# Optimization experiments

Measured on AMD Instinct MI355X. Metric: run time of the kernel, lower is better.

The kernel has to match this reference:

```python
import jax, jax.numpy as jnp
import numpy as np

B = 256          # batchSize
KNEG = 4096      # K negatives
D = 128          # inputSize
N = 1000000      # outputSize (memory bank rows)
T = 0.07
MOM = 0.5
STDV = 1.0 / np.sqrt(D / 3.0)


def setup_inputs() -> dict:
    key = jax.random.key(0)
    k1, k2, k3, k4, k5, k6 = jax.random.split(key, 6)
    ab = jax.random.normal(k1, (B, D), dtype=jnp.float32)
    l = jax.random.normal(k2, (B, D), dtype=jnp.float32)
    ss = jax.random.normal(k3, (B, D), dtype=jnp.float32)
    # memory bank initialized uniform in [-stdv, stdv] like the torch buffer
    memory_ab = jax.random.uniform(k4, (N, D), dtype=jnp.float32) * (2 * STDV) - STDV
    idx = jax.random.randint(k5, (B, KNEG + 1), 0, N)
    y = jax.random.randint(k6, (B,), 0, N)
    idx = idx.at[:, 0].set(y)  # positive sample in column 0
    return {"ab": ab, "l": l, "ss": ss, "memory_ab": memory_ab,
            "idx": idx, "y": y}


def reference(ab, l, ss, memory_ab, idx, y):
    # gather: [B, K+1, D]; detached in the original (no grad to the bank)
    w = jax.lax.stop_gradient(memory_ab[idx])
    # three batched dot-product scores against the same gathered weights
    out_l = jnp.einsum('bkd,bd->bk', w, l)[..., None] / T
    out_ss = jnp.einsum('bkd,bd->bk', w, ss)[..., None] / T
    out_orig = jnp.einsum('bkd,bd->bk', w, ab)[..., None] / T
    out = jnp.stack([out_orig, out_l, out_ss])  # [3, B, K+1, 1]
    # momentum scatter-update of the memory bank (no_grad in original)
    ab_pos = memory_ab[y] * MOM + ab * (1.0 - MOM)
    ab_norm = jnp.sqrt(jnp.sum(ab_pos * ab_pos, axis=1, keepdims=True))
    new_memory_ab = jax.lax.stop_gradient(memory_ab.at[y].set(ab_pos / ab_norm))
    return out, new_memory_ab
```

## Files before the change

kernel.cpp:

```cpp
#include <hip/hip_runtime.h>
#include <math.h>

constexpr int Bc   = 256;
constexpr int KP1  = 4097;
constexpr int Dc   = 128;
constexpr int NROW = 1000000;
constexpr float MOM = 0.5f;
constexpr float Tc  = 0.07f;

__global__ __launch_bounds__(256) void copy_mem_kernel(const float4* __restrict__ src,
                                                       float4* __restrict__ dst,
                                                       int n4) {
    int i = blockIdx.x * 256 + threadIdx.x;
    const int stride = gridDim.x * 256;
    for (; i < n4; i += stride) dst[i] = src[i];
}

__global__ __launch_bounds__(64) void scatter_kernel(const float* __restrict__ memory,
                                                     const float* __restrict__ ab,
                                                     const int* __restrict__ y,
                                                     float* __restrict__ out_mem) {
    const int b = blockIdx.x;
    const int row = y[b];
    for (int b2 = b + 1; b2 < Bc; ++b2)
        if (y[b2] == row) return;

    const int lane = threadIdx.x;
    float2 m = *(const float2*)(memory + (size_t)row * Dc + lane * 2);
    float2 a = *(const float2*)(ab + b * Dc + lane * 2);
    float v0 = m.x * MOM + a.x * (1.0f - MOM);
    float v1 = m.y * MOM + a.y * (1.0f - MOM);
    float s = v0 * v0 + v1 * v1;
#pragma unroll
    for (int off = 32; off; off >>= 1) s += __shfl_xor(s, off);
    const float inv = 1.0f / sqrtf(s);
    float2 o;
    o.x = v0 * inv;
    o.y = v1 * inv;
    *(float2*)(out_mem + (size_t)row * Dc + lane * 2) = o;
}

__global__ __launch_bounds__(256) void gather_dot_kernel(
    const float* __restrict__ memory,
    const float* __restrict__ ab,
    const float* __restrict__ l,
    const float* __restrict__ ss,
    const int* __restrict__ idx,
    float* __restrict__ out) {
    const int b    = blockIdx.x;
    const int lane = threadIdx.x & 63;
    const int wid  = (threadIdx.x >> 6) + (blockIdx.y << 2);
    const int nw   = gridDim.y << 2;
    const int g    = lane >> 3;
    const int sub  = lane & 7;

    float4 qa[4], ql[4], qs[4];
#pragma unroll
    for (int it = 0; it < 4; ++it) {
        const int d = it * 32 + sub * 4;
        qa[it] = *(const float4*)(ab + b * Dc + d);
        ql[it] = *(const float4*)(l + b * Dc + d);
        qs[it] = *(const float4*)(ss + b * Dc + d);
    }
    const int* idxb = idx + (size_t)b * KP1;
    const size_t out_b = (size_t)b * KP1;
    const size_t plane = (size_t)Bc * KP1;

    for (int k0 = wid * 8; k0 < KP1; k0 += nw * 8) {
        const int k = k0 + g;
        const int kc = (k < KP1) ? k : (KP1 - 1);
        const int row = idxb[kc];
        const float* wrow = memory + (size_t)row * Dc;
        float sa = 0.f, sl = 0.f, s2 = 0.f;
#pragma unroll
        for (int it = 0; it < 4; ++it) {
            const float4 w = *(const float4*)(wrow + it * 32 + sub * 4);
            sa += w.x * qa[it].x + w.y * qa[it].y + w.z * qa[it].z + w.w * qa[it].w;
            sl += w.x * ql[it].x + w.y * ql[it].y + w.z * ql[it].z + w.w * ql[it].w;
            s2 += w.x * qs[it].x + w.y * qs[it].y + w.z * qs[it].z + w.w * qs[it].w;
        }
#pragma unroll
        for (int off = 1; off < 8; off <<= 1) {
            sa += __shfl_xor(sa, off);
            sl += __shfl_xor(sl, off);
            s2 += __shfl_xor(s2, off);
        }
        if (sub == 0 && k < KP1) {
            out[0 * plane + out_b + k] = sa / Tc;
            out[1 * plane + out_b + k] = sl / Tc;
            out[2 * plane + out_b + k] = s2 / Tc;
        }
    }
}

extern "C" void kernel_launch(void* const* d_in, const int* in_sizes, int n_in,
                              void* d_out, int out_size, void* d_ws, size_t ws_size,
                              hipStream_t stream) {
    const float* ab     = (const float*)d_in[0];
    const float* l      = (const float*)d_in[1];
    const float* ss     = (const float*)d_in[2];
    const float* memory = (const float*)d_in[3];
    const int*   idx    = (const int*)d_in[4];
    const int*   y      = (const int*)d_in[5];

    float* out     = (float*)d_out;
    float* out_mem = out + (size_t)3 * Bc * KP1;

    const int n4 = (NROW * Dc) / 4;
    copy_mem_kernel<<<dim3(2048), dim3(256), 0, stream>>>(
        (const float4*)memory, (float4*)out_mem, n4);
    scatter_kernel<<<dim3(Bc), dim3(64), 0, stream>>>(memory, ab, y, out_mem);
    gather_dot_kernel<<<dim3(Bc, 16), dim3(256), 0, stream>>>(memory, ab, l, ss, idx, out);
}
```

Baseline: 313.6 us.

## Invert gather into per-row bucket index and fuse dot products into bank copy

Builds a per-memory-row bucket list of (b,k) references using atomics in workspace, then streams the whole memory bank once, copying each row and computing the dot products for every reference to that row. Rows with more than the bucket capacity go to an overflow list that a separate kernel processes. The intent is to avoid re-reading about a million gathered rows at random in addition to the full bank copy. In exchange it adds zeroing and atomic index-build passes over workspace, a serial per-row loop with divergent query loads, and a dependency on the workspace being large enough, with the old path kept as a fallback.

```diff
diff --git a/kernel.cpp b/kernel.cpp
--- a/kernel.cpp
+++ b/kernel.cpp
@@ -8,12 +8,126 @@
 constexpr float MOM = 0.5f;
 constexpr float Tc  = 0.07f;
 
-__global__ __launch_bounds__(256) void copy_mem_kernel(const float4* __restrict__ src,
-                                                       float4* __restrict__ dst,
-                                                       int n4) {
+constexpr int CAP   = 8;
+constexpr int OVCAP = 8192;
+
+constexpr size_t WS_CNT    = 0;
+constexpr size_t WS_OVCNT  = WS_CNT + NROW;
+constexpr size_t WS_OV     = WS_OVCNT + 1;
+constexpr size_t WS_SLOTS  = WS_OV + OVCAP;
+constexpr size_t WS_NEEDED = (WS_SLOTS + (size_t)NROW * CAP) * sizeof(int);
+
+__global__ __launch_bounds__(256) void zero_kernel(int* __restrict__ p, int n) {
     int i = blockIdx.x * 256 + threadIdx.x;
     const int stride = gridDim.x * 256;
-    for (; i < n4; i += stride) dst[i] = src[i];
+    for (; i < n; i += stride) p[i] = 0;
+}
+
+__global__ __launch_bounds__(256) void build_index_kernel(
+    const int* __restrict__ idx, int* __restrict__ cnt, int* __restrict__ slots,
+    int* __restrict__ ovcnt, int* __restrict__ ov) {
+    int i = blockIdx.x * 256 + threadIdx.x;
+    const int total = Bc * KP1;
+    const int stride = gridDim.x * 256;
+    for (; i < total; i += stride) {
+        const int row = idx[i];
+        const int b = i / KP1;
+        const int k = i - b * KP1;
+        const int e = (b << 13) | k;
+        const int c = atomicAdd(&cnt[row], 1);
+        if (c < CAP) {
+            slots[(size_t)row * CAP + c] = e;
+        } else {
+            const int o = atomicAdd(ovcnt, 1);
+            if (o < OVCAP) ov[o] = e;
+        }
+    }
+}
+
+__global__ __launch_bounds__(256) void fused_copy_dot_kernel(
+    const float* __restrict__ memory,
+    const float* __restrict__ ab, const float* __restrict__ l,
+    const float* __restrict__ ss,
+    const int* __restrict__ cnt, const int* __restrict__ slots,
+    float* __restrict__ out, float* __restrict__ out_mem) {
+    const int lane = threadIdx.x & 63;
+    const int half = lane >> 5;
+    const int sub  = lane & 31;
+    const int gw   = blockIdx.x * 4 + (threadIdx.x >> 6);
+    const int nw   = gridDim.x * 4;
+    const size_t plane = (size_t)Bc * KP1;
+    const float invT = 1.0f / Tc;
+
+    for (int rp = gw; rp < NROW / 2; rp += nw) {
+        const int row = rp * 2 + half;
+        const size_t off = (size_t)row * Dc + sub * 4;
+        const float4 w = *(const float4*)(memory + off);
+        *(float4*)(out_mem + off) = w;
+
+        int c = cnt[row];
+        if (c > CAP) c = CAP;
+        for (int j = 0; j < c; ++j) {
+            const int e = slots[(size_t)row * CAP + j];
+            const int b = e >> 13;
+            const int k = e & 8191;
+            const float4 qa = *(const float4*)(ab + b * Dc + sub * 4);
+            const float4 ql = *(const float4*)(l  + b * Dc + sub * 4);
+            const float4 qs = *(const float4*)(ss + b * Dc + sub * 4);
+            float sa = w.x * qa.x + w.y * qa.y + w.z * qa.z + w.w * qa.w;
+            float sl = w.x * ql.x + w.y * ql.y + w.z * ql.z + w.w * ql.w;
+            float s2 = w.x * qs.x + w.y * qs.y + w.z * qs.z + w.w * qs.w;
+#pragma unroll
+            for (int o = 16; o; o >>= 1) {
+                sa += __shfl_xor(sa, o);
+                sl += __shfl_xor(sl, o);
+                s2 += __shfl_xor(s2, o);
+            }
+            if (sub == 0) {
+                const size_t ob = (size_t)b * KP1 + k;
+                out[0 * plane + ob] = sa * invT;
+                out[1 * plane + ob] = sl * invT;
+                out[2 * plane + ob] = s2 * invT;
+            }
+        }
+    }
+}
+
+__global__ __launch_bounds__(64) void overflow_dot_kernel(
+    const float* __restrict__ memory,
+    const float* __restrict__ ab, const float* __restrict__ l,
+    const float* __restrict__ ss, const int* __restrict__ idx,
+    const int* __restrict__ ovcnt, const int* __restrict__ ov,
+    float* __restrict__ out) {
+    int n = *ovcnt;
+    if (n > OVCAP) n = OVCAP;
+    const int lane = threadIdx.x;
+    const size_t plane = (size_t)Bc * KP1;
+    const float invT = 1.0f / Tc;
+    for (int i = blockIdx.x; i < n; i += gridDim.x) {
+        const int e = ov[i];
+        const int b = e >> 13;
+        const int k = e & 8191;
+        const int row = idx[(size_t)b * KP1 + k];
+        const float2 w = *(const float2*)(memory + (size_t)row * Dc + lane * 2);
+        const float2 qa = *(const float2*)(ab + b * Dc + lane * 2);
+        const float2 ql = *(const float2*)(l  + b * Dc + lane * 2);
+        const float2 qs = *(const float2*)(ss + b * Dc + lane * 2);
+        float sa = w.x * qa.x + w.y * qa.y;
+        float sl = w.x * ql.x + w.y * ql.y;
+        float s2 = w.x * qs.x + w.y * qs.y;
+#pragma unroll
+        for (int o = 32; o; o >>= 1) {
+            sa += __shfl_xor(sa, o);
+            sl += __shfl_xor(sl, o);
+            s2 += __shfl_xor(s2, o);
+        }
+        if (lane == 0) {
+            const size_t ob = (size_t)b * KP1 + k;
+            out[0 * plane + ob] = sa * invT;
+            out[1 * plane + ob] = sl * invT;
+            out[2 * plane + ob] = s2 * invT;
+        }
+    }
 }
 
 __global__ __launch_bounds__(64) void scatter_kernel(const float* __restrict__ memory,
@@ -38,6 +152,14 @@
     o.x = v0 * inv;
     o.y = v1 * inv;
     *(float2*)(out_mem + (size_t)row * Dc + lane * 2) = o;
+}
+
+__global__ __launch_bounds__(256) void copy_mem_kernel(const float4* __restrict__ src,
+                                                       float4* __restrict__ dst,
+                                                       int n4) {
+    int i = blockIdx.x * 256 + threadIdx.x;
+    const int stride = gridDim.x * 256;
+    for (; i < n4; i += stride) dst[i] = src[i];
 }
 
 __global__ __launch_bounds__(256) void gather_dot_kernel(
@@ -106,9 +228,25 @@
     float* out     = (float*)d_out;
     float* out_mem = out + (size_t)3 * Bc * KP1;
 
-    const int n4 = (NROW * Dc) / 4;
-    copy_mem_kernel<<<dim3(2048), dim3(256), 0, stream>>>(
-        (const float4*)memory, (float4*)out_mem, n4);
-    scatter_kernel<<<dim3(Bc), dim3(64), 0, stream>>>(memory, ab, y, out_mem);
-    gather_dot_kernel<<<dim3(Bc, 16), dim3(256), 0, stream>>>(memory, ab, l, ss, idx, out);
-}
+    if (ws_size >= WS_NEEDED) {
+        int* wsi   = (int*)d_ws;
+        int* cnt   = wsi + WS_CNT;
+        int* ovcnt = wsi + WS_OVCNT;
+        int* ov    = wsi + WS_OV;
+        int* slots = wsi + WS_SLOTS;
+
+        zero_kernel<<<dim3(512), dim3(256), 0, stream>>>(cnt, NROW + 1);
+        build_index_kernel<<<dim3(1024), dim3(256), 0, stream>>>(idx, cnt, slots, ovcnt, ov);
+        fused_copy_dot_kernel<<<dim3(2048), dim3(256), 0, stream>>>(
+            memory, ab, l, ss, cnt, slots, out, out_mem);
+        overflow_dot_kernel<<<dim3(64), dim3(64), 0, stream>>>(
+            memory, ab, l, ss, idx, ovcnt, ov, out);
+        scatter_kernel<<<dim3(Bc), dim3(64), 0, stream>>>(memory, ab, y, out_mem);
+    } else {
+        const int n4 = (NROW * Dc) / 4;
+        copy_mem_kernel<<<dim3(2048), dim3(256), 0, stream>>>(
+            (const float4*)memory, (float4*)out_mem, n4);
+        scatter_kernel<<<dim3(Bc), dim3(64), 0, stream>>>(memory, ab, y, out_mem);
+        gather_dot_kernel<<<dim3(Bc, 16), dim3(256), 0, stream>>>(memory, ab, l, ss, idx, out);
+    }
+}
```

Measured after the change: 471.7 us. 1.5x slower.

## Fuse bank copy and gather-dot into one heterogeneous kernel running concurrently

Applied to the files above, without the earlier changes.

Merges the memory-bank copy and the gather-dot-product into a single launch: the first 512 blocks do the 512 MB bank copy with 4-way unrolled float4 loads, and the other 512 blocks do the gather dots at 2 blocks per batch row. The aim is to overlap the bandwidth-bound copy with the latency-bound random gathers and drop one launch. The trade-off is far fewer gather blocks than before (512 instead of 4096), so gather parallelism drops and the two halves compete for HBM bandwidth. The division by T is also replaced by a multiply by 1/T, which can change results in the last bit.

```diff
diff --git a/kernel.cpp b/kernel.cpp
--- a/kernel.cpp
+++ b/kernel.cpp
@@ -8,12 +8,82 @@
 constexpr float MOM = 0.5f;
 constexpr float Tc  = 0.07f;
 
-__global__ __launch_bounds__(256) void copy_mem_kernel(const float4* __restrict__ src,
-                                                       float4* __restrict__ dst,
-                                                       int n4) {
-    int i = blockIdx.x * 256 + threadIdx.x;
-    const int stride = gridDim.x * 256;
-    for (; i < n4; i += stride) dst[i] = src[i];
+constexpr int NCOPY = 512;
+constexpr int NGATH = 512;
+
+__global__ __launch_bounds__(256) void combo_kernel(
+    const float* __restrict__ memory,
+    const float* __restrict__ ab,
+    const float* __restrict__ l,
+    const float* __restrict__ ss,
+    const int* __restrict__ idx,
+    float* __restrict__ out,
+    float* __restrict__ out_mem) {
+    if (blockIdx.x < NCOPY) {
+        const float4* __restrict__ src = (const float4*)memory;
+        float4* __restrict__ dst = (float4*)out_mem;
+        const int n4 = NROW * Dc / 4;
+        const int S  = NCOPY * 256;
+        int i = blockIdx.x * 256 + threadIdx.x;
+        for (; i + 3 * S < n4; i += 4 * S) {
+            float4 a0 = src[i];
+            float4 a1 = src[i + S];
+            float4 a2 = src[i + 2 * S];
+            float4 a3 = src[i + 3 * S];
+            dst[i]         = a0;
+            dst[i + S]     = a1;
+            dst[i + 2 * S] = a2;
+            dst[i + 3 * S] = a3;
+        }
+        for (; i < n4; i += S) dst[i] = src[i];
+    } else {
+        const int gb   = blockIdx.x - NCOPY;
+        const int b    = gb >> 1;
+        const int lane = threadIdx.x & 63;
+        const int wid  = ((gb & 1) << 2) + (threadIdx.x >> 6);
+        const int nw   = 8;
+        const int g    = lane >> 3;
+        const int sub  = lane & 7;
+
+        float4 qa[4], ql[4], qs[4];
+#pragma unroll
+        for (int it = 0; it < 4; ++it) {
+            const int d = it * 32 + sub * 4;
+            qa[it] = *(const float4*)(ab + b * Dc + d);
+            ql[it] = *(const float4*)(l  + b * Dc + d);
+            qs[it] = *(const float4*)(ss + b * Dc + d);
+        }
+        const int* idxb = idx + (size_t)b * KP1;
+        const size_t out_b = (size_t)b * KP1;
+        const size_t plane = (size_t)Bc * KP1;
+        const float invT = 1.0f / Tc;
+
+        for (int k0 = wid * 8; k0 < KP1; k0 += nw * 8) {
+            const int k = k0 + g;
+            const int kc = (k < KP1) ? k : (KP1 - 1);
+            const int row = idxb[kc];
+            const float* wrow = memory + (size_t)row * Dc;
+            float sa = 0.f, sl = 0.f, s2 = 0.f;
+#pragma unroll
+            for (int it = 0; it < 4; ++it) {
+                const float4 w = *(const float4*)(wrow + it * 32 + sub * 4);
+                sa += w.x * qa[it].x + w.y * qa[it].y + w.z * qa[it].z + w.w * qa[it].w;
+                sl += w.x * ql[it].x + w.y * ql[it].y + w.z * ql[it].z + w.w * ql[it].w;
+                s2 += w.x * qs[it].x + w.y * qs[it].y + w.z * qs[it].z + w.w * qs[it].w;
+            }
+#pragma unroll
+            for (int off = 1; off < 8; off <<= 1) {
+                sa += __shfl_xor(sa, off);
+                sl += __shfl_xor(sl, off);
+                s2 += __shfl_xor(s2, off);
+            }
+            if (sub == 0 && k < KP1) {
+                out[0 * plane + out_b + k] = sa * invT;
+                out[1 * plane + out_b + k] = sl * invT;
+                out[2 * plane + out_b + k] = s2 * invT;
+            }
+        }
+    }
 }
 
 __global__ __launch_bounds__(64) void scatter_kernel(const float* __restrict__ memory,
@@ -40,59 +110,6 @@
     *(float2*)(out_mem + (size_t)row * Dc + lane * 2) = o;
 }
 
-__global__ __launch_bounds__(256) void gather_dot_kernel(
-    const float* __restrict__ memory,
-    const float* __restrict__ ab,
-    const float* __restrict__ l,
-    const float* __restrict__ ss,
-    const int* __restrict__ idx,
-    float* __restrict__ out) {
-    const int b    = blockIdx.x;
-    const int lane = threadIdx.x & 63;
-    const int wid  = (threadIdx.x >> 6) + (blockIdx.y << 2);
-    const int nw   = gridDim.y << 2;
-    const int g    = lane >> 3;
-    const int sub  = lane & 7;
-
-    float4 qa[4], ql[4], qs[4];
-#pragma unroll
-    for (int it = 0; it < 4; ++it) {
-        const int d = it * 32 + sub * 4;
-        qa[it] = *(const float4*)(ab + b * Dc + d);
-        ql[it] = *(const float4*)(l + b * Dc + d);
-        qs[it] = *(const float4*)(ss + b * Dc + d);
-    }
-    const int* idxb = idx + (size_t)b * KP1;
-    const size_t out_b = (size_t)b * KP1;
-    const size_t plane = (size_t)Bc * KP1;
-
-    for (int k0 = wid * 8; k0 < KP1; k0 += nw * 8) {
-        const int k = k0 + g;
-        const int kc = (k < KP1) ? k : (KP1 - 1);
-        const int row = idxb[kc];
-        const float* wrow = memory + (size_t)row * Dc;
-        float sa = 0.f, sl = 0.f, s2 = 0.f;
-#pragma unroll
-        for (int it = 0; it < 4; ++it) {
-            const float4 w = *(const float4*)(wrow + it * 32 + sub * 4);
-            sa += w.x * qa[it].x + w.y * qa[it].y + w.z * qa[it].z + w.w * qa[it].w;
-            sl += w.x * ql[it].x + w.y * ql[it].y + w.z * ql[it].z + w.w * ql[it].w;
-            s2 += w.x * qs[it].x + w.y * qs[it].y + w.z * qs[it].z + w.w * qs[it].w;
-        }
-#pragma unroll
-        for (int off = 1; off < 8; off <<= 1) {
-            sa += __shfl_xor(sa, off);
-            sl += __shfl_xor(sl, off);
-            s2 += __shfl_xor(s2, off);
-        }
-        if (sub == 0 && k < KP1) {
-            out[0 * plane + out_b + k] = sa / Tc;
-            out[1 * plane + out_b + k] = sl / Tc;
-            out[2 * plane + out_b + k] = s2 / Tc;
-        }
-    }
-}
-
 extern "C" void kernel_launch(void* const* d_in, const int* in_sizes, int n_in,
                               void* d_out, int out_size, void* d_ws, size_t ws_size,
                               hipStream_t stream) {
@@ -106,9 +123,7 @@
     float* out     = (float*)d_out;
     float* out_mem = out + (size_t)3 * Bc * KP1;
 
-    const int n4 = (NROW * Dc) / 4;
-    copy_mem_kernel<<<dim3(2048), dim3(256), 0, stream>>>(
-        (const float4*)memory, (float4*)out_mem, n4);
+    combo_kernel<<<dim3(NCOPY + NGATH), dim3(256), 0, stream>>>(
+        memory, ab, l, ss, idx, out, out_mem);
     scatter_kernel<<<dim3(Bc), dim3(64), 0, stream>>>(memory, ab, y, out_mem);
-    gather_dot_kernel<<<dim3(Bc, 16), dim3(256), 0, stream>>>(memory, ab, l, ss, idx, out);
 }
```

Result: slower. 352.2 us (+12.3%).
